# Optimization experiments

Measured on AMD Instinct MI355X. Metric: run time of the kernel, lower is better.

## Reference

```python
import jax, jax.numpy as jnp
import numpy as np

DIM = 1024
NUM_HEADS = 16
HEAD_DIM = DIM // NUM_HEADS  # 64
KSIZE = 5


def setup_inputs() -> dict:
    key = jax.random.key(0)
    ks = jax.random.split(key, 7)
    B, N, C = 4, 4096, DIM
    s = 0.02
    return {
        "x": jax.random.normal(ks[0], (B, N, C), dtype=jnp.float32),
        "Wq": jax.random.normal(ks[1], (C, C), dtype=jnp.float32) * s,
        "Wkv": jax.random.normal(ks[2], (C, 2 * C), dtype=jnp.float32) * s,
        "Wproj": jax.random.normal(ks[3], (C, C), dtype=jnp.float32) * s,
        "bproj": jnp.zeros((C,), dtype=jnp.float32),
        "dwc_w": jax.random.normal(ks[4], (HEAD_DIM, 1, KSIZE, KSIZE), dtype=jnp.float32) * s,
        "dwc_b": jnp.zeros((HEAD_DIM,), dtype=jnp.float32),
    }


def reference(x, Wq, Wkv, Wproj, bproj, dwc_w, dwc_b):
    B, N, C = x.shape
    h, d = NUM_HEADS, HEAD_DIM
    H = W = int(N ** 0.5)

    q = x @ Wq                       # [B,N,C]
    kv_lin = x @ Wkv                 # [B,N,2C]
    k, v = kv_lin[..., :C], kv_lin[..., C:]

    eps = 1e-6
    q = jax.nn.relu(q) + eps
    k = jax.nn.relu(k) + eps

    # split heads -> [B,h,N,d]
    q = q.reshape(B, N, h, d).transpose(0, 2, 1, 3)
    k = k.reshape(B, N, h, d).transpose(0, 2, 1, 3)
    v = v.reshape(B, N, h, d).transpose(0, 2, 1, 3)

    k_mean = k.mean(axis=2)                                   # [B,h,d]
    z = 1.0 / (jnp.einsum('bhnd,bhd->bhn', q, k_mean) + eps)  # [B,h,N]

    # (k^T * N^-0.5) @ (v * N^-0.5) = k^T v / N
    kv = jnp.einsum('bhnd,bhne->bhde', k, v) / N              # [B,h,d,d]
    att = jnp.einsum('bhnd,bhde->bhne', q, kv) * z[..., None]  # [B,h,N,d]
    att = att.transpose(0, 2, 1, 3).reshape(B, N, C)

    # depthwise conv enhancement on v
    v_img = v.reshape(B * h, H, W, d).transpose(0, 3, 1, 2)   # [B*h,d,H,W]
    conv = jax.lax.conv_general_dilated(
        v_img, dwc_w, window_strides=(1, 1), padding='SAME',
        feature_group_count=d,
        dimension_numbers=('NCHW', 'OIHW', 'NCHW'))
    conv = conv + dwc_b[None, :, None, None]
    conv = conv.reshape(B, C, N).transpose(0, 2, 1)           # [B,N,C]

    out = (att + conv) @ Wproj + bproj
    return out
```

## Files before the change

### kernel.cpp

```cpp
#include <hip/hip_runtime.h>
#include <stdint.h>

typedef unsigned short u16;

#define B_   4
#define N_   4096
#define C_   1024
#define NT_  (B_*N_)
#define HW_  64

typedef __attribute__((ext_vector_type(8))) short bf16x8;
typedef __attribute__((ext_vector_type(4))) float f32x4;

__device__ __forceinline__ float b2f(u16 s) {
    union { uint32_t u; float f; } x; x.u = ((uint32_t)s) << 16; return x.f;
}
__device__ __forceinline__ u16 f2b(float f) {
    union { float f; uint32_t u; } x; x.f = f;
    uint32_t u = x.u;
    return (u16)((u + 0x7FFFu + ((u >> 16) & 1u)) >> 16);
}
__device__ __forceinline__ float lo2f(uint32_t u) {
    union { uint32_t u; float f; } x; x.u = u << 16; return x.f;
}
__device__ __forceinline__ float hi2f(uint32_t u) {
    union { uint32_t u; float f; } x; x.u = u & 0xFFFF0000u; return x.f;
}
__device__ __forceinline__ void unpack8(uint4 v, float* f) {
    f[0] = lo2f(v.x); f[1] = hi2f(v.x); f[2] = lo2f(v.y); f[3] = hi2f(v.y);
    f[4] = lo2f(v.z); f[5] = hi2f(v.z); f[6] = lo2f(v.w); f[7] = hi2f(v.w);
}

__global__ void detect_fmt(const u16* __restrict__ x, int* __restrict__ flag)
{
    __shared__ int smax[256];
    const int t = threadIdx.x;
    int m = 0;
    for (int i = t; i < 2048; i += 256) {
        int e = (x[2 * i] >> 7) & 0xFF;
        m = m > e ? m : e;
    }
    smax[t] = m;
    __syncthreads();
    for (int s = 128; s > 0; s >>= 1) {
        if (t < s) smax[t] = smax[t] > smax[t + s] ? smax[t] : smax[t + s];
        __syncthreads();
    }
    if (t == 0) flag[0] = (smax[0] >= 0x90) ? 1 : 0;
}

__global__ void zero_f32(float* p, int n) {
    int i = blockIdx.x * 256 + threadIdx.x;
    if (i < n) p[i] = 0.f;
}

__global__ __launch_bounds__(256)
void convert_x(const void* __restrict__ x, u16* __restrict__ xb,
               const int* __restrict__ flag)
{
    const int fmt = flag[0];
    const size_t total = (size_t)NT_ * C_ / 8;
    const size_t stride = (size_t)gridDim.x * 256;
    size_t i = (size_t)blockIdx.x * 256 + threadIdx.x;
    if (fmt) {
        for (; i < total; i += stride) {
            const float4* p = (const float4*)x + i * 2;
            float4 a = p[0], b = p[1];
            union { uint4 v; u16 s[8]; } o;
            o.s[0] = f2b(a.x); o.s[1] = f2b(a.y); o.s[2] = f2b(a.z); o.s[3] = f2b(a.w);
            o.s[4] = f2b(b.x); o.s[5] = f2b(b.y); o.s[6] = f2b(b.z); o.s[7] = f2b(b.w);
            ((uint4*)xb)[i] = o.v;
        }
    } else {
        for (; i < total; i += stride)
            ((uint4*)xb)[i] = ((const uint4*)x)[i];
    }
}

__global__ __launch_bounds__(256)
void transpose_w(const void* __restrict__ W, u16* __restrict__ WT,
                 const int* __restrict__ flag, int ldw, int col0, int Kdim)
{
    __shared__ u16 tile[64][65];
    const int fmt = flag[0];
    const int n0 = blockIdx.x * 64, k0 = blockIdx.y * 64;
    const int t = threadIdx.x;
    const int c = t & 63, rg = t >> 6;
    #pragma unroll 4
    for (int i = 0; i < 16; ++i) {
        int r = rg * 16 + i;
        size_t gi = (size_t)(k0 + r) * ldw + col0 + n0 + c;
        tile[r][c] = fmt ? f2b(((const float*)W)[gi]) : ((const u16*)W)[gi];
    }
    __syncthreads();
    #pragma unroll 4
    for (int i = 0; i < 16; ++i) {
        int r = rg * 16 + i;
        WT[(size_t)(n0 + r) * Kdim + k0 + c] = tile[c][r];
    }
}

template<int RELU, int BIAS, int AEXT, int CEXT>
__global__ __launch_bounds__(256)
void gemm_mfma(const void* __restrict__ A, const u16* __restrict__ BT,
               void* __restrict__ Cout, const void* __restrict__ bias,
               const int* __restrict__ flag, int K, int ldc)
{
    __shared__ u16 As[AEXT ? 1 : 4][128 * 32];
    __shared__ u16 Bs[AEXT ? 1 : 4][128 * 32];
    const int fmt = flag[0];
    const int t    = threadIdx.x;
    const int lane = t & 63;
    const int w    = t >> 6;
    const int wm   = w >> 1, wn = w & 1;
    const int quad = lane >> 4;
    const int l16  = lane & 15;

    int bid = blockIdx.y * gridDim.x + blockIdx.x;
    const int nwg = gridDim.x * gridDim.y;
    if ((nwg & 7) == 0)
        bid = (bid & 7) * (nwg >> 3) + (bid >> 3);
    const int j0 = (bid % gridDim.x) * 128;
    const int m0 = (bid / gridDim.x) * 128;

    const int srow = lane >> 2;
    const int gseg = ((lane & 3) ^ ((lane >> 3) & 3)) * 8;

    f32x4 acc[4][4] = {};

    if (AEXT) {
        for (int k0 = 0; k0 < K; k0 += 32) {
            if (fmt) {
                #pragma unroll
                for (int i = 0; i < 2; ++i) {
                    const int r0 = w * 32 + i * 16;
                    const float* gp = (const float*)A + (size_t)(m0 + r0 + srow) * K + k0 + gseg;
                    float4 f0 = *(const float4*)gp;
                    float4 f1 = *(const float4*)(gp + 4);
                    union { bf16x8 v; u16 s[8]; } o;
                    o.s[0] = f2b(f0.x); o.s[1] = f2b(f0.y); o.s[2] = f2b(f0.z); o.s[3] = f2b(f0.w);
                    o.s[4] = f2b(f1.x); o.s[5] = f2b(f1.y); o.s[6] = f2b(f1.z); o.s[7] = f2b(f1.w);
                    *(bf16x8*)&As[0][(r0 + srow) * 32 + (lane & 3) * 8] = o.v;
                }
            } else {
                #pragma unroll
                for (int i = 0; i < 2; ++i) {
                    const int r0 = w * 32 + i * 16;
                    const u16* gp = (const u16*)A + (size_t)(m0 + r0 + srow) * K + k0 + gseg;
                    __builtin_amdgcn_global_load_lds(
                        (const __attribute__((address_space(1))) void*)gp,
                        (__attribute__((address_space(3))) void*)&As[0][r0 * 32], 16, 0, 0);
                }
            }
            #pragma unroll
            for (int i = 0; i < 2; ++i) {
                const int r0 = w * 32 + i * 16;
                const u16* gp = BT + (size_t)(j0 + r0 + srow) * K + k0 + gseg;
                __builtin_amdgcn_global_load_lds(
                    (const __attribute__((address_space(1))) void*)gp,
                    (__attribute__((address_space(3))) void*)&Bs[0][r0 * 32], 16, 0, 0);
            }
            __syncthreads();

            bf16x8 af[4], bfr[4];
            #pragma unroll
            for (int mt = 0; mt < 4; ++mt) {
                const int r = wm * 64 + mt * 16 + l16;
                const int slot = quad ^ ((r >> 1) & 3);
                af[mt] = *(const bf16x8*)&As[0][r * 32 + slot * 8];
            }
            #pragma unroll
            for (int nt = 0; nt < 4; ++nt) {
                const int r = wn * 64 + nt * 16 + l16;
                const int slot = quad ^ ((r >> 1) & 3);
                bfr[nt] = *(const bf16x8*)&Bs[0][r * 32 + slot * 8];
            }
            #pragma unroll
            for (int mt = 0; mt < 4; ++mt)
                #pragma unroll
                for (int nt = 0; nt < 4; ++nt)
                    acc[mt][nt] = __builtin_amdgcn_mfma_f32_16x16x32_bf16(
                        af[mt], bfr[nt], acc[mt][nt], 0, 0, 0);
            __syncthreads();
        }
    } else {
        auto stage = [&](int buf, int tile) {
            const int kk = tile * 32;
            #pragma unroll
            for (int i = 0; i < 2; ++i) {
                const int r0 = w * 32 + i * 16;
                const u16* gp = (const u16*)A + (size_t)(m0 + r0 + srow) * K + kk + gseg;
                __builtin_amdgcn_global_load_lds(
                    (const __attribute__((address_space(1))) void*)gp,
                    (__attribute__((address_space(3))) void*)&As[buf][r0 * 32], 16, 0, 0);
            }
            #pragma unroll
            for (int i = 0; i < 2; ++i) {
                const int r0 = w * 32 + i * 16;
                const u16* gp = BT + (size_t)(j0 + r0 + srow) * K + kk + gseg;
                __builtin_amdgcn_global_load_lds(
                    (const __attribute__((address_space(1))) void*)gp,
                    (__attribute__((address_space(3))) void*)&Bs[buf][r0 * 32], 16, 0, 0);
            }
        };
        auto compute = [&](int buf) {
            bf16x8 af[4], bfr[4];
            #pragma unroll
            for (int mt = 0; mt < 4; ++mt) {
                const int r = wm * 64 + mt * 16 + l16;
                const int slot = quad ^ ((r >> 1) & 3);
                af[mt] = *(const bf16x8*)&As[buf][r * 32 + slot * 8];
            }
            #pragma unroll
            for (int nt = 0; nt < 4; ++nt) {
                const int r = wn * 64 + nt * 16 + l16;
                const int slot = quad ^ ((r >> 1) & 3);
                bfr[nt] = *(const bf16x8*)&Bs[buf][r * 32 + slot * 8];
            }
            __builtin_amdgcn_s_setprio(1);
            #pragma unroll
            for (int mt = 0; mt < 4; ++mt)
                #pragma unroll
                for (int nt = 0; nt < 4; ++nt)
                    acc[mt][nt] = __builtin_amdgcn_mfma_f32_16x16x32_bf16(
                        af[mt], bfr[nt], acc[mt][nt], 0, 0, 0);
            __builtin_amdgcn_s_setprio(0);
        };
        #define GBAR() do {                                   \
            __builtin_amdgcn_sched_barrier(0);                \
            asm volatile("s_barrier" ::: "memory");           \
            __builtin_amdgcn_sched_barrier(0);                \
        } while (0)

        const int nsteps = K >> 5;
        stage(0, 0); stage(1, 1); stage(2, 2);

        int tt = 0;
        for (; tt + 4 < nsteps; tt += 4) {
            stage(3, tt + 3);
            asm volatile("s_waitcnt vmcnt(12)" ::: "memory");
            GBAR(); compute(0); GBAR();
            stage(0, tt + 4);
            asm volatile("s_waitcnt vmcnt(12)" ::: "memory");
            GBAR(); compute(1); GBAR();
            stage(1, tt + 5);
            asm volatile("s_waitcnt vmcnt(12)" ::: "memory");
            GBAR(); compute(2); GBAR();
            stage(2, tt + 6);
            asm volatile("s_waitcnt vmcnt(12)" ::: "memory");
            GBAR(); compute(3); GBAR();
        }
        stage(3, tt + 3);
        asm volatile("s_waitcnt vmcnt(12)" ::: "memory");
        GBAR(); compute(0); GBAR();
        asm volatile("s_waitcnt vmcnt(8)" ::: "memory");
        GBAR(); compute(1); GBAR();
        asm volatile("s_waitcnt vmcnt(4)" ::: "memory");
        GBAR(); compute(2); GBAR();
        asm volatile("s_waitcnt vmcnt(0)" ::: "memory");
        GBAR(); compute(3);
        #undef GBAR
    }

    #pragma unroll
    for (int mt = 0; mt < 4; ++mt) {
        #pragma unroll
        for (int nt = 0; nt < 4; ++nt) {
            const int col = j0 + wn * 64 + nt * 16 + l16;
            float bv = 0.f;
            if (BIAS) bv = fmt ? ((const float*)bias)[col] : b2f(((const u16*)bias)[col]);
            #pragma unroll
            for (int r = 0; r < 4; ++r) {
                const int row = m0 + wm * 64 + mt * 16 + quad * 4 + r;
                float v = acc[mt][nt][r];
                if (BIAS) v += bv;
                if (RELU) v = fmaxf(v, 0.f) + 1e-6f;
                if (CEXT && fmt) ((float*)Cout)[(size_t)row * ldc + col] = v;
                else             ((u16*)Cout)[(size_t)row * ldc + col] = f2b(v);
            }
        }
    }
}

template<int RELU, int BIAS, int AEXT, int CEXT>
__global__ __launch_bounds__(256)
void gemm_any(const void* __restrict__ A, const void* __restrict__ Bm,
              void* __restrict__ Cout, const void* __restrict__ bias,
              const int* __restrict__ flag,
              int M, int K, int ldb, int bcol0, int ldc)
{
    const int fmt = flag[0];
    __shared__ float As[16][128];
    __shared__ float Bs[16][128];
    const int t  = threadIdx.x;
    const int tx = t & 15, ty = t >> 4;
    const int m0 = blockIdx.y * 128;
    const int j0 = blockIdx.x * 128;
    const int la_row = t >> 1;
    const int la_k   = (t & 1) * 8;
    const int lb_k   = t >> 4;
    const int lb_j   = (t & 15) * 8;

    float acc[8][8];
    #pragma unroll
    for (int i = 0; i < 8; ++i)
        #pragma unroll
        for (int j = 0; j < 8; ++j) acc[i][j] = 0.f;

    for (int k0 = 0; k0 < K; k0 += 16) {
        float af[8], bfv[8];
        if (AEXT && fmt) {
            const float* ap = (const float*)A + (size_t)(m0 + la_row) * K + k0 + la_k;
            float4 a0 = *(const float4*)ap;
            float4 a1 = *(const float4*)(ap + 4);
            af[0] = a0.x; af[1] = a0.y; af[2] = a0.z; af[3] = a0.w;
            af[4] = a1.x; af[5] = a1.y; af[6] = a1.z; af[7] = a1.w;
        } else {
            uint4 av = *(const uint4*)((const u16*)A + (size_t)(m0 + la_row) * K + k0 + la_k);
            unpack8(av, af);
        }
        if (fmt) {
            const float* bp = (const float*)Bm + (size_t)(k0 + lb_k) * ldb + bcol0 + j0 + lb_j;
            float4 b0 = *(const float4*)bp;
            float4 b1 = *(const float4*)(bp + 4);
            bfv[0] = b0.x; bfv[1] = b0.y; bfv[2] = b0.z; bfv[3] = b0.w;
            bfv[4] = b1.x; bfv[5] = b1.y; bfv[6] = b1.z; bfv[7] = b1.w;
        } else {
            uint4 bv = *(const uint4*)((const u16*)Bm + (size_t)(k0 + lb_k) * ldb + bcol0 + j0 + lb_j);
            unpack8(bv, bfv);
        }
        __syncthreads();
        #pragma unroll
        for (int i = 0; i < 8; ++i) As[la_k + i][la_row] = af[i];
        *(float4*)&Bs[lb_k][lb_j]     = make_float4(bfv[0], bfv[1], bfv[2], bfv[3]);
        *(float4*)&Bs[lb_k][lb_j + 4] = make_float4(bfv[4], bfv[5], bfv[6], bfv[7]);
        __syncthreads();
        #pragma unroll
        for (int kk = 0; kk < 16; ++kk) {
            float a[8], b[8];
            *(float4*)&a[0] = *(const float4*)&As[kk][ty * 8];
            *(float4*)&a[4] = *(const float4*)&As[kk][ty * 8 + 4];
            *(float4*)&b[0] = *(const float4*)&Bs[kk][tx * 8];
            *(float4*)&b[4] = *(const float4*)&Bs[kk][tx * 8 + 4];
            #pragma unroll
            for (int i = 0; i < 8; ++i)
                #pragma unroll
                for (int j = 0; j < 8; ++j)
                    acc[i][j] += a[i] * b[j];
        }
    }

    #pragma unroll
    for (int i = 0; i < 8; ++i) {
        const int m = m0 + ty * 8 + i;
        float vals[8];
        #pragma unroll
        for (int j = 0; j < 8; ++j) {
            float v = acc[i][j];
            if (BIAS) {
                const int bi = j0 + tx * 8 + j;
                v += fmt ? ((const float*)bias)[bi] : b2f(((const u16*)bias)[bi]);
            }
            if (RELU) v = fmaxf(v, 0.f) + 1e-6f;
            vals[j] = v;
        }
        if (CEXT && fmt) {
            float* cp = (float*)Cout + (size_t)m * ldc + j0 + tx * 8;
            *(float4*)cp       = make_float4(vals[0], vals[1], vals[2], vals[3]);
            *(float4*)(cp + 4) = make_float4(vals[4], vals[5], vals[6], vals[7]);
        } else {
            union { uint4 v; u16 s[8]; } o;
            #pragma unroll
            for (int j = 0; j < 8; ++j) o.s[j] = f2b(vals[j]);
            *(uint4*)((u16*)Cout + (size_t)m * ldc + j0 + tx * 8) = o.v;
        }
    }
}

__global__ __launch_bounds__(256)
void kmean_kernel(const u16* __restrict__ k, float* __restrict__ km)
{
    const int c  = blockIdx.x * 256 + threadIdx.x;
    const int b  = blockIdx.y;
    const int nc = blockIdx.z;
    const u16* p = k + ((size_t)b * N_ + nc * 256) * C_ + c;
    float s = 0.f;
    for (int n = 0; n < 256; ++n) s += b2f(p[(size_t)n * C_]);
    atomicAdd(&km[b * C_ + c], s * (1.0f / N_));
}

__global__ __launch_bounds__(256)
void kv_atomic(const u16* __restrict__ k, const u16* __restrict__ v,
               float* __restrict__ kvh)
{
    __shared__ float kk[4][64];
    __shared__ float vv[4][64];
    const int bh = blockIdx.x;
    const int ch = blockIdx.y;
    const int b = bh >> 4, h = bh & 15;
    const int t = threadIdx.x;
    const int e = t & 63, d0 = (t >> 6) * 16;
    const int lr = t >> 6, lc = t & 63;
    const int n0 = ch * 512;
    float acc[16];
    #pragma unroll
    for (int i = 0; i < 16; ++i) acc[i] = 0.f;

    for (int nb = 0; nb < 512; nb += 4) {
        size_t base = ((size_t)(b * N_ + n0 + nb + lr)) * C_ + h * 64 + lc;
        float kf = b2f(k[base]);
        float vf = b2f(v[base]);
        __syncthreads();
        kk[lr][lc] = kf;
        vv[lr][lc] = vf;
        __syncthreads();
        #pragma unroll
        for (int r = 0; r < 4; ++r) {
            float ve = vv[r][e];
            #pragma unroll
            for (int i = 0; i < 16; ++i) acc[i] += kk[r][d0 + i] * ve;
        }
    }
    float* dst = kvh + (size_t)bh * 4096;
    #pragma unroll
    for (int i = 0; i < 16; ++i)
        atomicAdd(&dst[(d0 + i) * 64 + e], acc[i] * (1.0f / N_));
}

__global__ __launch_bounds__(256)
void att_kernel(const u16* __restrict__ q, const float* __restrict__ kvh,
                const float* __restrict__ kmean, u16* __restrict__ y)
{
    __shared__ float kvs[64 * 64];
    __shared__ float qs[64 * 68];
    __shared__ float kmv[64];
    __shared__ float zs[64];
    const int bh = blockIdx.y;
    const int b = bh >> 4, h = bh & 15;
    const int n0 = blockIdx.x * 64;
    const int t = threadIdx.x;
    const int e = t & 63, rg = t >> 6;

    const float4* kvsrc4 = (const float4*)(kvh + (size_t)bh * 4096);
    #pragma unroll
    for (int i = 0; i < 4; ++i)
        *(float4*)&kvs[(i * 256 + t) * 4] = kvsrc4[i * 256 + t];
    if (t < 64) kmv[t] = kmean[b * C_ + h * 64 + t];
    #pragma unroll
    for (int ii = 0; ii < 2; ++ii) {
        int i = ii * 256 + t;
        int r = i >> 3, c8 = (i & 7) * 8;
        uint4 v = *(const uint4*)&q[((size_t)(b * N_ + n0 + r)) * C_ + h * 64 + c8];
        float f[8];
        unpack8(v, f);
        #pragma unroll
        for (int j = 0; j < 8; ++j) qs[r * 68 + c8 + j] = f[j];
    }
    __syncthreads();

    float kvr[64];
    #pragma unroll
    for (int d = 0; d < 64; ++d) kvr[d] = kvs[d * 64 + e];

    if (t < 64) {
        float s = 1e-6f;
        #pragma unroll
        for (int d = 0; d < 64; ++d) s += qs[t * 68 + d] * kmv[d];
        zs[t] = 1.0f / s;
    }
    __syncthreads();

    for (int rr = 0; rr < 16; ++rr) {
        int r = rg * 16 + rr;
        float acc = 0.f;
        #pragma unroll
        for (int d = 0; d < 64; ++d) acc += qs[r * 68 + d] * kvr[d];
        y[((size_t)(b * N_ + n0 + r)) * C_ + h * 64 + e] = f2b(acc * zs[r]);
    }
}

__global__ __launch_bounds__(256)
void conv_add(const u16* __restrict__ v, const void* __restrict__ w,
              const void* __restrict__ wb, u16* __restrict__ y,
              const int* __restrict__ flag)
{
    __shared__ float wt[25][64];
    __shared__ float bl[64];
    const int fmt = flag[0];
    const int t = threadIdx.x;
    for (int i = t; i < 1600; i += 256) {
        const int tap = i >> 6, c = i & 63;
        const int src = c * 25 + tap;
        wt[tap][c] = fmt ? ((const float*)w)[src] : b2f(((const u16*)w)[src]);
    }
    if (t < 64)
        bl[t] = fmt ? ((const float*)wb)[t] : b2f(((const u16*)wb)[t]);
    __syncthreads();

    const size_t gid = (size_t)blockIdx.x * 256 + t;
    const int cg = (int)(gid & 127);
    const int n  = (int)((gid >> 7) & 4095);
    const int b  = (int)(gid >> 19);
    const int c0 = cg * 8;
    const int cb = c0 & 63;
    const int yp = n >> 6, xp = n & 63;

    float acc[8];
    #pragma unroll
    for (int j = 0; j < 8; ++j) acc[j] = bl[cb + j];

    const u16* vbase = v + (size_t)b * N_ * C_ + c0;
    #pragma unroll
    for (int dy = 0; dy < 5; ++dy) {
        const int yy = yp + dy - 2;
        if (yy < 0 || yy >= HW_) continue;
        #pragma unroll
        for (int dx = 0; dx < 5; ++dx) {
            const int xx = xp + dx - 2;
            if (xx < 0 || xx >= HW_) continue;
            uint4 pv = *(const uint4*)(vbase + (size_t)(yy * HW_ + xx) * C_);
            float f[8];
            unpack8(pv, f);
            const int tap = dy * 5 + dx;
            float4 w0 = *(const float4*)&wt[tap][cb];
            float4 w1 = *(const float4*)&wt[tap][cb + 4];
            acc[0] += w0.x * f[0]; acc[1] += w0.y * f[1];
            acc[2] += w0.z * f[2]; acc[3] += w0.w * f[3];
            acc[4] += w1.x * f[4]; acc[5] += w1.y * f[5];
            acc[6] += w1.z * f[6]; acc[7] += w1.w * f[7];
        }
    }

    uint4 yv = *(const uint4*)(y + gid * 8);
    float yf[8];
    unpack8(yv, yf);
    union { uint4 v4; u16 s[8]; } o;
    #pragma unroll
    for (int j = 0; j < 8; ++j) o.s[j] = f2b(yf[j] + acc[j]);
    *(uint4*)(y + gid * 8) = o.v4;
}

extern "C" void kernel_launch(void* const* d_in, const int* in_sizes, int n_in,
                              void* d_out, int out_size, void* d_ws, size_t ws_size,
                              hipStream_t stream)
{
    const void* x     = d_in[0];
    const void* Wq    = d_in[1];
    const void* Wkv   = d_in[2];
    const void* Wproj = d_in[3];
    const void* bproj = d_in[4];
    const void* dwc_w = d_in[5];
    const void* dwc_b = d_in[6];

    char* ws = (char*)d_ws;
    const size_t MI = 1024 * 1024;
    const size_t NEED_FAST = 35 * MI + 17 * 1024;
    const size_t OUT_ELEMS = (size_t)NT_ * C_;

    if (ws_size >= NEED_FAST && (size_t)out_size >= OUT_ELEMS) {
        u16*   vbuf  = (u16*)ws;
        u16*   WT    = (u16*)(ws + 32 * MI);
        float* kvh   = (float*)(ws + 34 * MI);
        float* kmean = (float*)(ws + 35 * MI);
        int*   flag  = (int*)(ws + 35 * MI + 16 * 1024);
        u16*   xb    = (u16*)d_out;
        u16*   kq    = (u16*)d_out + (size_t)NT_ * C_;
        u16*   ybuf  = (u16*)ws;

        detect_fmt<<<1, 256, 0, stream>>>((const u16*)x, flag);
        zero_f32<<<dim3(1040), 256, 0, stream>>>(kvh, 266240);
        convert_x<<<dim3(2048), 256, 0, stream>>>(x, xb, flag);

        transpose_w<<<dim3(16, 16), 256, 0, stream>>>(Wkv, WT, flag, 2 * C_, C_, C_);
        gemm_mfma<0, 0, 0, 0><<<dim3(8, 128), 256, 0, stream>>>(xb, WT, vbuf, nullptr, flag, C_, C_);
        transpose_w<<<dim3(16, 16), 256, 0, stream>>>(Wkv, WT, flag, 2 * C_, 0, C_);
        gemm_mfma<1, 0, 0, 0><<<dim3(8, 128), 256, 0, stream>>>(xb, WT, kq, nullptr, flag, C_, C_);

        kmean_kernel<<<dim3(4, B_, 16), 256, 0, stream>>>(kq, kmean);
        kv_atomic<<<dim3(64, 8), 256, 0, stream>>>(kq, vbuf, kvh);

        transpose_w<<<dim3(16, 16), 256, 0, stream>>>(Wq, WT, flag, C_, 0, C_);
        gemm_mfma<1, 0, 0, 0><<<dim3(8, 128), 256, 0, stream>>>(xb, WT, kq, nullptr, flag, C_, C_);

        att_kernel<<<dim3(64, 64), 256, 0, stream>>>(kq, kvh, kmean, kq);
        conv_add<<<dim3(8192), 256, 0, stream>>>(vbuf, dwc_w, dwc_b, kq, flag);

        hipMemcpyAsync(ws, kq, (size_t)NT_ * C_ * sizeof(u16), hipMemcpyDeviceToDevice, stream);
        transpose_w<<<dim3(16, 16), 256, 0, stream>>>(Wproj, WT, flag, C_, 0, C_);
        gemm_mfma<0, 1, 0, 1><<<dim3(8, 128), 256, 0, stream>>>(ybuf, WT, d_out, bproj, flag, C_, C_);
    } else if (ws_size >= NEED_FAST) {
        u16*   vbuf  = (u16*)ws;
        u16*   WT    = (u16*)(ws + 32 * MI);
        float* kvh   = (float*)(ws + 34 * MI);
        float* kmean = (float*)(ws + 35 * MI);
        int*   flag  = (int*)(ws + 35 * MI + 16 * 1024);
        u16*   kq    = (u16*)d_out;
        u16*   ybuf  = (u16*)ws;

        detect_fmt<<<1, 256, 0, stream>>>((const u16*)x, flag);
        zero_f32<<<dim3(1040), 256, 0, stream>>>(kvh, 266240);

        transpose_w<<<dim3(16, 16), 256, 0, stream>>>(Wkv, WT, flag, 2 * C_, C_, C_);
        gemm_mfma<0, 0, 1, 0><<<dim3(8, 128), 256, 0, stream>>>(x, WT, vbuf, nullptr, flag, C_, C_);
        transpose_w<<<dim3(16, 16), 256, 0, stream>>>(Wkv, WT, flag, 2 * C_, 0, C_);
        gemm_mfma<1, 0, 1, 0><<<dim3(8, 128), 256, 0, stream>>>(x, WT, kq, nullptr, flag, C_, C_);

        kmean_kernel<<<dim3(4, B_, 16), 256, 0, stream>>>(kq, kmean);
        kv_atomic<<<dim3(64, 8), 256, 0, stream>>>(kq, vbuf, kvh);

        transpose_w<<<dim3(16, 16), 256, 0, stream>>>(Wq, WT, flag, C_, 0, C_);
        gemm_mfma<1, 0, 1, 0><<<dim3(8, 128), 256, 0, stream>>>(x, WT, kq, nullptr, flag, C_, C_);

        att_kernel<<<dim3(64, 64), 256, 0, stream>>>(kq, kvh, kmean, kq);
        conv_add<<<dim3(8192), 256, 0, stream>>>(vbuf, dwc_w, dwc_b, kq, flag);

        hipMemcpyAsync(ws, d_out, (size_t)NT_ * C_ * sizeof(u16), hipMemcpyDeviceToDevice, stream);
        transpose_w<<<dim3(16, 16), 256, 0, stream>>>(Wproj, WT, flag, C_, 0, C_);
        gemm_mfma<0, 1, 0, 1><<<dim3(8, 128), 256, 0, stream>>>(ybuf, WT, d_out, bproj, flag, C_, C_);
    } else {
        u16*   vbuf  = (u16*)ws;
        float* kmean = (float*)(ws + 32 * MI);
        float* kvh   = (float*)(ws + 32 * MI + 16 * 1024);
        int*   flag  = (int*)(ws + 32 * MI + 16 * 1024 + 1 * MI);
        u16*   kq    = (u16*)d_out;
        u16*   ybuf  = (u16*)ws;

        detect_fmt<<<1, 256, 0, stream>>>((const u16*)x, flag);
        zero_f32<<<dim3(1040), 256, 0, stream>>>(kmean, 266240);

        gemm_any<0, 0, 1, 0><<<dim3(8, 128), 256, 0, stream>>>(x, Wkv, vbuf, nullptr, flag, NT_, C_, 2 * C_, C_, C_);
        gemm_any<1, 0, 1, 0><<<dim3(8, 128), 256, 0, stream>>>(x, Wkv, kq,   nullptr, flag, NT_, C_, 2 * C_, 0,  C_);

        kmean_kernel<<<dim3(4, B_, 16), 256, 0, stream>>>(kq, kmean);
        kv_atomic<<<dim3(64, 8), 256, 0, stream>>>(kq, vbuf, kvh);

        gemm_any<1, 0, 1, 0><<<dim3(8, 128), 256, 0, stream>>>(x, Wq, kq, nullptr, flag, NT_, C_, C_, 0, C_);

        att_kernel<<<dim3(64, 64), 256, 0, stream>>>(kq, kvh, kmean, kq);
        conv_add<<<dim3(8192), 256, 0, stream>>>(vbuf, dwc_w, dwc_b, kq, flag);

        hipMemcpyAsync(ws, d_out, (size_t)NT_ * C_ * sizeof(u16), hipMemcpyDeviceToDevice, stream);
        gemm_any<0, 1, 0, 1><<<dim3(8, 128), 256, 0, stream>>>(ybuf, Wproj, d_out, bproj, flag, NT_, C_, C_, 0, C_);
    }
}
```

Measured before the change: 574.1 us.

## Fuse k-mean reduction into kv_atomic and vectorize its loads with prefetch

Removes the separate kmean_kernel and computes the per-head column sums of k inside kv_atomic, reusing the k values already loaded for the k^T v product. The kv kernel now loads 8 bf16 values per thread with 128-bit loads, stages 32 rows per iteration instead of 4, and prefetches the next tile into registers. This saves one pass over k and cuts the barrier count per block by a factor of eight, at the cost of more shared memory and registers.

```diff
diff --git a/kernel.cpp b/kernel.cpp
--- a/kernel.cpp
+++ b/kernel.cpp
@@ -378,53 +378,70 @@
 }
 
 __global__ __launch_bounds__(256)
-void kmean_kernel(const u16* __restrict__ k, float* __restrict__ km)
-{
-    const int c  = blockIdx.x * 256 + threadIdx.x;
-    const int b  = blockIdx.y;
-    const int nc = blockIdx.z;
-    const u16* p = k + ((size_t)b * N_ + nc * 256) * C_ + c;
-    float s = 0.f;
-    for (int n = 0; n < 256; ++n) s += b2f(p[(size_t)n * C_]);
-    atomicAdd(&km[b * C_ + c], s * (1.0f / N_));
-}
-
-__global__ __launch_bounds__(256)
 void kv_atomic(const u16* __restrict__ k, const u16* __restrict__ v,
-               float* __restrict__ kvh)
-{
-    __shared__ float kk[4][64];
-    __shared__ float vv[4][64];
+               float* __restrict__ kvh, float* __restrict__ km)
+{
+    __shared__ float kk[32][64];
+    __shared__ float vv[32][64];
     const int bh = blockIdx.x;
     const int ch = blockIdx.y;
     const int b = bh >> 4, h = bh & 15;
     const int t = threadIdx.x;
     const int e = t & 63, d0 = (t >> 6) * 16;
-    const int lr = t >> 6, lc = t & 63;
+    const int lr = t >> 3;
+    const int lc = (t & 7) * 8;
     const int n0 = ch * 512;
+
     float acc[16];
     #pragma unroll
     for (int i = 0; i < 16; ++i) acc[i] = 0.f;
-
-    for (int nb = 0; nb < 512; nb += 4) {
-        size_t base = ((size_t)(b * N_ + n0 + nb + lr)) * C_ + h * 64 + lc;
-        float kf = b2f(k[base]);
-        float vf = b2f(v[base]);
+    float ksum[8];
+    #pragma unroll
+    for (int j = 0; j < 8; ++j) ksum[j] = 0.f;
+
+    const u16* kbase = k + ((size_t)(b * N_ + n0 + lr)) * C_ + h * 64 + lc;
+    const u16* vbase = v + ((size_t)(b * N_ + n0 + lr)) * C_ + h * 64 + lc;
+
+    uint4 kreg = *(const uint4*)kbase;
+    uint4 vreg = *(const uint4*)vbase;
+
+    for (int rd = 0; rd < 16; ++rd) {
+        float kf[8], vf[8];
+        unpack8(kreg, kf);
+        unpack8(vreg, vf);
+        if (rd + 1 < 16) {
+            kreg = *(const uint4*)(kbase + (size_t)(rd + 1) * 32 * C_);
+            vreg = *(const uint4*)(vbase + (size_t)(rd + 1) * 32 * C_);
+        }
+        #pragma unroll
+        for (int j = 0; j < 8; ++j) ksum[j] += kf[j];
         __syncthreads();
-        kk[lr][lc] = kf;
-        vv[lr][lc] = vf;
+        #pragma unroll
+        for (int j = 0; j < 8; ++j) { kk[lr][lc + j] = kf[j]; vv[lr][lc + j] = vf[j]; }
         __syncthreads();
         #pragma unroll
-        for (int r = 0; r < 4; ++r) {
+        for (int r = 0; r < 32; ++r) {
             float ve = vv[r][e];
             #pragma unroll
             for (int i = 0; i < 16; ++i) acc[i] += kk[r][d0 + i] * ve;
         }
     }
+
     float* dst = kvh + (size_t)bh * 4096;
     #pragma unroll
     for (int i = 0; i < 16; ++i)
         atomicAdd(&dst[(d0 + i) * 64 + e], acc[i] * (1.0f / N_));
+
+    __syncthreads();
+    #pragma unroll
+    for (int j = 0; j < 8; ++j) kk[lr][lc + j] = ksum[j];
+    __syncthreads();
+    if (t < 64) {
+        float s = 0.f;
+        #pragma unroll
+        for (int r = 0; r < 32; ++r) s += kk[r][t];
+        atomicAdd(&km[b * C_ + h * 64 + t], s * (1.0f / N_));
+    }
 }
 
 __global__ __launch_bounds__(256)
@@ -576,8 +593,7 @@
         transpose_w<<<dim3(16, 16), 256, 0, stream>>>(Wkv, WT, flag, 2 * C_, 0, C_);
         gemm_mfma<1, 0, 0, 0><<<dim3(8, 128), 256, 0, stream>>>(xb, WT, kq, nullptr, flag, C_, C_);
 
-        kmean_kernel<<<dim3(4, B_, 16), 256, 0, stream>>>(kq, kmean);
-        kv_atomic<<<dim3(64, 8), 256, 0, stream>>>(kq, vbuf, kvh);
+        kv_atomic<<<dim3(64, 8), 256, 0, stream>>>(kq, vbuf, kvh, kmean);
 
         transpose_w<<<dim3(16, 16), 256, 0, stream>>>(Wq, WT, flag, C_, 0, C_);
         gemm_mfma<1, 0, 0, 0><<<dim3(8, 128), 256, 0, stream>>>(xb, WT, kq, nullptr, flag, C_, C_);
@@ -605,8 +621,7 @@
         transpose_w<<<dim3(16, 16), 256, 0, stream>>>(Wkv, WT, flag, 2 * C_, 0, C_);
         gemm_mfma<1, 0, 1, 0><<<dim3(8, 128), 256, 0, stream>>>(x, WT, kq, nullptr, flag, C_, C_);
 
-        kmean_kernel<<<dim3(4, B_, 16), 256, 0, stream>>>(kq, kmean);
-        kv_atomic<<<dim3(64, 8), 256, 0, stream>>>(kq, vbuf, kvh);
+        kv_atomic<<<dim3(64, 8), 256, 0, stream>>>(kq, vbuf, kvh, kmean);
 
         transpose_w<<<dim3(16, 16), 256, 0, stream>>>(Wq, WT, flag, C_, 0, C_);
         gemm_mfma<1, 0, 1, 0><<<dim3(8, 128), 256, 0, stream>>>(x, WT, kq, nullptr, flag, C_, C_);
@@ -631,8 +646,7 @@
         gemm_any<0, 0, 1, 0><<<dim3(8, 128), 256, 0, stream>>>(x, Wkv, vbuf, nullptr, flag, NT_, C_, 2 * C_, C_, C_);
         gemm_any<1, 0, 1, 0><<<dim3(8, 128), 256, 0, stream>>>(x, Wkv, kq,   nullptr, flag, NT_, C_, 2 * C_, 0,  C_);
 
-        kmean_kernel<<<dim3(4, B_, 16), 256, 0, stream>>>(kq, kmean);
-        kv_atomic<<<dim3(64, 8), 256, 0, stream>>>(kq, vbuf, kvh);
+        kv_atomic<<<dim3(64, 8), 256, 0, stream>>>(kq, vbuf, kvh, kmean);
 
         gemm_any<1, 0, 1, 0><<<dim3(8, 128), 256, 0, stream>>>(x, Wq, kq, nullptr, flag, NT_, C_, C_, 0, C_);
 
```

After: 529.9 us. 1.08x faster.
